# Kernel optimization log

Measured on AMD Instinct MI355X. Metric: run time of the kernel, lower is better.

The kernel has to match this reference:

```python
import jax, jax.numpy as jnp
import numpy as np

N, D = 131072, 512

def setup_inputs() -> dict:
    key = jax.random.key(0)
    k1, k2, k3 = jax.random.split(key, 3)
    feature = jax.random.normal(k1, (N, D), dtype=jnp.float32)
    mean = jax.random.normal(k2, (D,), dtype=jnp.float32)
    inverse_cov = jax.random.normal(k3, (D, D), dtype=jnp.float32)
    return {"feature": feature, "mean": mean, "inverse_cov": inverse_cov}

def reference(feature, mean, inverse_cov):
    # zero_f: [N, D]
    zero_f = feature - mean
    # diag(zero_f @ inv_cov @ zero_f.T) == rowwise quadratic form,
    # computed without the NxN intermediate: (zero_f @ inv_cov * zero_f).sum(-1)
    quad = jnp.einsum('nd,de,ne->n', zero_f, inverse_cov, zero_f)
    return jnp.mean(quad)
```

## Files before the change

kernel.cpp:

```cpp
#include <hip/hip_runtime.h>
#include <hip/hip_bf16.h>
#include <stdint.h>


typedef __attribute__((ext_vector_type(8))) short short8;
typedef __attribute__((ext_vector_type(4))) short short4v;
typedef __attribute__((ext_vector_type(4))) float floatx4;

static constexpr int NROWS = 131072;
static constexpr int DDIM  = 512;
static constexpr int AST   = 72;
static constexpr int SLOT  = 128 * AST;

__device__ __forceinline__ short f2bf(float f) {
  __bf16 b = (__bf16)f;
  return __builtin_bit_cast(short, b);
}
__device__ __forceinline__ float bf2f(short s) {
  __bf16 b = __builtin_bit_cast(__bf16, s);
  return (float)b;
}

__global__ __launch_bounds__(512) void maha_zero(float* __restrict__ s_ws,
                                                 float* __restrict__ out) {
  s_ws[threadIdx.x] = 0.0f;
  if (threadIdx.x == 0) out[0] = 0.0f;
}

__global__ __launch_bounds__(256, 2) void maha_gram(const float* __restrict__ F,
                                                    const float* __restrict__ C,
                                                    float* __restrict__ s_ws,
                                                    float* __restrict__ out) {
  __shared__ short As[2 * SLOT];
  __shared__ short Bs[2 * SLOT];
  __shared__ float sred[512];
  __shared__ float red[4];

  static const int TI[10] = {0,0,0,0,1,1,1,2,2,3};
  static const int TJ[10] = {0,1,2,3,1,2,3,2,3,3};

  const int bid  = blockIdx.x;
  const int gg   = bid / 80;
  const int rr   = bid % 80;
  const int slab = gg * 8 + (rr & 7);
  const int tile = rr >> 3;
  const int ti = TI[tile], tj = TJ[tile];
  const bool diag = (ti == tj);

  const int th = threadIdx.x;
  const int half = th >> 7;
  const int t2   = th & 127;
  const int tp   = t2 & 31;
  const int tn   = t2 >> 5;
  const int colbase = 128 * (half ? tj : ti);
  short* mybuf = half ? Bs : As;

  const int noff = (tn + (tp >> 2)) & 3;
  const int tphi = tp >> 4;
  const int gsw  = 8 * (tp & 7);

  const float* gbase = F + (size_t)slab * 1024 * DDIM + colbase + 4 * tp;

  floatx4 v[4][4];

  auto loadG = [&](int c) {
#pragma unroll
    for (int k = 0; k < 4; k++) {
      const int kq = k ^ tphi;
      const int nb = 4 * kq + noff;
      const float* p = gbase + (size_t)(c * 64 + 4 * nb) * DDIM;
#pragma unroll
      for (int nn = 0; nn < 4; nn++)
        v[k][nn] = *(const floatx4*)(p + nn * DDIM);
    }
  };

  float s_part[4] = {0.f, 0.f, 0.f, 0.f};
  const bool sacc = diag && (half == 0);

  auto cvtwrite = [&](int slot) {
#pragma unroll
    for (int k = 0; k < 4; k++) {
      const int kq = k ^ tphi;
      const int nb = 4 * kq + noff;
      const int naddr = (4 * nb) ^ gsw;
#pragma unroll
      for (int dd = 0; dd < 4; dd++) {
        short4v pk;
        pk[0] = f2bf(v[k][0][dd]); pk[1] = f2bf(v[k][1][dd]);
        pk[2] = f2bf(v[k][2][dd]); pk[3] = f2bf(v[k][3][dd]);
        *(short4v*)&mybuf[slot * SLOT + (4 * tp + dd) * AST + naddr] = pk;
        if (sacc)
          s_part[dd] += bf2f(pk[0]) + bf2f(pk[1]) + bf2f(pk[2]) + bf2f(pk[3]);
      }
    }
  };

  const int wave = th >> 6, lane = th & 63;
  const int wm = wave >> 1, wn = wave & 1;
  const int l15 = lane & 15, quad = lane >> 4;

  int aoff[4], swA[4], boff[4], swB[4];
#pragma unroll
  for (int mi = 0; mi < 4; mi++) {
    const int d = wm * 64 + mi * 16 + l15;
    aoff[mi] = d * AST;  swA[mi] = 8 * ((d >> 2) & 7);
    const int e = wn * 64 + mi * 16 + l15;
    boff[mi] = e * AST;  swB[mi] = 8 * ((e >> 2) & 7);
  }

  floatx4 acc[4][4];
#pragma unroll
  for (int i = 0; i < 4; i++)
#pragma unroll
    for (int j = 0; j < 4; j++) acc[i][j] = floatx4{0.f, 0.f, 0.f, 0.f};

  loadG(0);
  cvtwrite(0);
  loadG(1);

#pragma unroll 2
  for (int c = 0; c < 16; ++c) {
    const int slot = c & 1;
    __syncthreads();
    short8 af[2][4], bfr[2][4];
#pragma unroll
    for (int ks = 0; ks < 2; ks++) {
#pragma unroll
      for (int mi = 0; mi < 4; mi++)
        af[ks][mi] = *(const short8*)&As[slot * SLOT + aoff[mi] +
                                         ((ks * 32 + quad * 8) ^ swA[mi])];
#pragma unroll
      for (int fj = 0; fj < 4; fj++)
        bfr[ks][fj] = *(const short8*)&Bs[slot * SLOT + boff[fj] +
                                          ((ks * 32 + quad * 8) ^ swB[fj])];
    }
    if (c < 15) cvtwrite(slot ^ 1);
    if (c < 14) loadG(c + 2);
#pragma unroll
    for (int ks = 0; ks < 2; ks++)
#pragma unroll
      for (int mi = 0; mi < 4; mi++)
#pragma unroll
        for (int fj = 0; fj < 4; fj++)
          acc[mi][fj] = __builtin_amdgcn_mfma_f32_16x16x32_bf16(
              af[ks][mi], bfr[ks][fj], acc[mi][fj], 0, 0, 0);
  }

  const int d0 = ti * 128, e0 = tj * 128;
  float psum = 0.f;
#pragma unroll
  for (int mi = 0; mi < 4; mi++) {
#pragma unroll
    for (int fj = 0; fj < 4; fj++) {
      const int dg = d0 + wm * 64 + mi * 16 + quad * 4;
      const int eg = e0 + wn * 64 + fj * 16 + l15;
#pragma unroll
      for (int r2 = 0; r2 < 4; r2++) {
        float wgt = C[(size_t)(dg + r2) * DDIM + eg];
        if (!diag) wgt += C[(size_t)eg * DDIM + dg + r2];
        psum += wgt * acc[mi][fj][r2];
      }
    }
  }

#pragma unroll
  for (int off = 32; off > 0; off >>= 1) psum += __shfl_down(psum, off);
  if (lane == 0) red[wave] = psum;
  if (sacc) {
#pragma unroll
    for (int dd = 0; dd < 4; dd++) sred[(4 * tp + dd) * 4 + tn] = s_part[dd];
  }
  __syncthreads();
  if (th == 0) {
    const float tot = red[0] + red[1] + red[2] + red[3];
    atomicAdd(out, tot * (1.0f / (float)NROWS));
  }
  if (diag && th < 128) {
    const float sd = sred[th * 4] + sred[th * 4 + 1] + sred[th * 4 + 2] + sred[th * 4 + 3];
    atomicAdd(&s_ws[ti * 128 + th], sd);
  }
}

__global__ __launch_bounds__(256) void maha_corr(const float* __restrict__ C,
                                                 const float* __restrict__ mu,
                                                 const float* __restrict__ s_ws,
                                                 float* __restrict__ out) {
  __shared__ float red[4];
  const int b = blockIdx.x;
  const int th = threadIdx.x;
  float cd[4], md[4];
#pragma unroll
  for (int dd = 0; dd < 4; dd++) {
    const int d = b * 4 + dd;
    md[dd] = mu[d];
    cd[dd] = s_ws[d] - 0.5f * (float)NROWS * md[dd];
  }
  float p = 0.f;
#pragma unroll
  for (int rep = 0; rep < 2; rep++) {
    const int e = th + rep * 256;
    const float me = mu[e];
    const float ce = s_ws[e] - 0.5f * (float)NROWS * me;
#pragma unroll
    for (int dd = 0; dd < 4; dd++)
      p += C[(size_t)(b * 4 + dd) * DDIM + e] * (cd[dd] * me + md[dd] * ce);
  }
  const int lane = th & 63, wave = th >> 6;
#pragma unroll
  for (int off = 32; off > 0; off >>= 1) p += __shfl_down(p, off);
  if (lane == 0) red[wave] = p;
  __syncthreads();
  if (th == 0)
    atomicAdd(out, -(red[0] + red[1] + red[2] + red[3]) * (1.0f / (float)NROWS));
}

extern "C" void kernel_launch(void* const* d_in, const int* in_sizes, int n_in,
                              void* d_out, int out_size, void* d_ws, size_t ws_size,
                              hipStream_t stream) {
  const float* feature = (const float*)d_in[0];
  const float* mean    = (const float*)d_in[1];
  const float* invcov  = (const float*)d_in[2];
  float* out = (float*)d_out;
  float* s_ws = (float*)d_ws;

  maha_zero<<<1, 512, 0, stream>>>(s_ws, out);
  maha_gram<<<1280, 256, 0, stream>>>(feature, invcov, s_ws, out);
  maha_corr<<<128, 256, 0, stream>>>(invcov, mean, s_ws, out);
}
```

Measured before the change: 426.3 us.

## Split K across waves with 512-thread blocks and reuse A tile on diagonal

The Gram-tile kernel moves to 512 threads per block. The extra waves split each 64-wide K chunk between wave pairs, so each wave issues half the MFMAs and half the LDS fragment loads per iteration, and per-thread staging registers are halved. On diagonal tiles the B half of the block skips its global loads and conversions and reads from the A buffer instead, which cuts redundant feature traffic. The cost is more threads per block, a reduction over 8 waves, and a higher occupancy target that may force register spilling.

```diff
diff --git a/kernel.cpp b/kernel.cpp
--- a/kernel.cpp
+++ b/kernel.cpp
@@ -27,14 +27,13 @@
   if (threadIdx.x == 0) out[0] = 0.0f;
 }
 
-__global__ __launch_bounds__(256, 2) void maha_gram(const float* __restrict__ F,
+__global__ __launch_bounds__(512, 4) void maha_gram(const float* __restrict__ F,
                                                     const float* __restrict__ C,
                                                     float* __restrict__ s_ws,
                                                     float* __restrict__ out) {
-  __shared__ short As[2 * SLOT];
-  __shared__ short Bs[2 * SLOT];
-  __shared__ float sred[512];
-  __shared__ float red[4];
+  __shared__ short ABs[4 * SLOT];
+  __shared__ float sred[1024];
+  __shared__ float red[8];
 
   static const int TI[10] = {0,0,0,0,1,1,1,2,2,3};
   static const int TJ[10] = {0,1,2,3,1,2,3,2,3,3};
@@ -48,26 +47,28 @@
   const bool diag = (ti == tj);
 
   const int th = threadIdx.x;
-  const int half = th >> 7;
-  const int t2   = th & 127;
+  const int half = th >> 8;
+  const int t2   = th & 255;
   const int tp   = t2 & 31;
   const int tn   = t2 >> 5;
   const int colbase = 128 * (half ? tj : ti);
-  short* mybuf = half ? Bs : As;
-
-  const int noff = (tn + (tp >> 2)) & 3;
-  const int tphi = tp >> 4;
+  short* mybuf = ABs + (half ? 2 * SLOT : 0);
+  const bool skipstage = diag && (half == 1);
+
+  const int tphi = (tp >> 4) & 1;
+  const int noff = (tn + (tp >> 2)) & 7;
   const int gsw  = 8 * (tp & 7);
 
   const float* gbase = F + (size_t)slab * 1024 * DDIM + colbase + 4 * tp;
 
-  floatx4 v[4][4];
+  floatx4 v[2][4];
 
   auto loadG = [&](int c) {
-#pragma unroll
-    for (int k = 0; k < 4; k++) {
+    if (skipstage) return;
+#pragma unroll
+    for (int k = 0; k < 2; k++) {
       const int kq = k ^ tphi;
-      const int nb = 4 * kq + noff;
+      const int nb = 8 * kq + noff;
       const float* p = gbase + (size_t)(c * 64 + 4 * nb) * DDIM;
 #pragma unroll
       for (int nn = 0; nn < 4; nn++)
@@ -79,10 +80,11 @@
   const bool sacc = diag && (half == 0);
 
   auto cvtwrite = [&](int slot) {
-#pragma unroll
-    for (int k = 0; k < 4; k++) {
+    if (skipstage) return;
+#pragma unroll
+    for (int k = 0; k < 2; k++) {
       const int kq = k ^ tphi;
-      const int nb = 4 * kq + noff;
+      const int nb = 8 * kq + noff;
       const int naddr = (4 * nb) ^ gsw;
 #pragma unroll
       for (int dd = 0; dd < 4; dd++) {
@@ -97,8 +99,14 @@
   };
 
   const int wave = th >> 6, lane = th & 63;
-  const int wm = wave >> 1, wn = wave & 1;
+  const int wk = wave & 1;
+  const int wm = (wave >> 1) & 1;
+  const int wn = (wave >> 2) & 1;
   const int l15 = lane & 15, quad = lane >> 4;
+  const int kcol = wk * 32 + quad * 8;
+
+  const short* Ard = ABs;
+  const short* Brd = ABs + (diag ? 0 : 2 * SLOT);
 
   int aoff[4], swA[4], boff[4], swB[4];
 #pragma unroll
@@ -123,28 +131,21 @@
   for (int c = 0; c < 16; ++c) {
     const int slot = c & 1;
     __syncthreads();
-    short8 af[2][4], bfr[2][4];
-#pragma unroll
-    for (int ks = 0; ks < 2; ks++) {
-#pragma unroll
-      for (int mi = 0; mi < 4; mi++)
-        af[ks][mi] = *(const short8*)&As[slot * SLOT + aoff[mi] +
-                                         ((ks * 32 + quad * 8) ^ swA[mi])];
-#pragma unroll
-      for (int fj = 0; fj < 4; fj++)
-        bfr[ks][fj] = *(const short8*)&Bs[slot * SLOT + boff[fj] +
-                                          ((ks * 32 + quad * 8) ^ swB[fj])];
-    }
+    short8 af[4], bfr[4];
+#pragma unroll
+    for (int mi = 0; mi < 4; mi++)
+      af[mi] = *(const short8*)&Ard[slot * SLOT + aoff[mi] + (kcol ^ swA[mi])];
+#pragma unroll
+    for (int fj = 0; fj < 4; fj++)
+      bfr[fj] = *(const short8*)&Brd[slot * SLOT + boff[fj] + (kcol ^ swB[fj])];
     if (c < 15) cvtwrite(slot ^ 1);
     if (c < 14) loadG(c + 2);
 #pragma unroll
-    for (int ks = 0; ks < 2; ks++)
-#pragma unroll
-      for (int mi = 0; mi < 4; mi++)
-#pragma unroll
-        for (int fj = 0; fj < 4; fj++)
-          acc[mi][fj] = __builtin_amdgcn_mfma_f32_16x16x32_bf16(
-              af[ks][mi], bfr[ks][fj], acc[mi][fj], 0, 0, 0);
+    for (int mi = 0; mi < 4; mi++)
+#pragma unroll
+      for (int fj = 0; fj < 4; fj++)
+        acc[mi][fj] = __builtin_amdgcn_mfma_f32_16x16x32_bf16(
+            af[mi], bfr[fj], acc[mi][fj], 0, 0, 0);
   }
 
   const int d0 = ti * 128, e0 = tj * 128;
@@ -169,15 +170,18 @@
   if (lane == 0) red[wave] = psum;
   if (sacc) {
 #pragma unroll
-    for (int dd = 0; dd < 4; dd++) sred[(4 * tp + dd) * 4 + tn] = s_part[dd];
+    for (int dd = 0; dd < 4; dd++) sred[(4 * tp + dd) * 8 + tn] = s_part[dd];
   }
   __syncthreads();
   if (th == 0) {
-    const float tot = red[0] + red[1] + red[2] + red[3];
+    const float tot = red[0] + red[1] + red[2] + red[3] +
+                      red[4] + red[5] + red[6] + red[7];
     atomicAdd(out, tot * (1.0f / (float)NROWS));
   }
   if (diag && th < 128) {
-    const float sd = sred[th * 4] + sred[th * 4 + 1] + sred[th * 4 + 2] + sred[th * 4 + 3];
+    float sd = 0.f;
+#pragma unroll
+    for (int j = 0; j < 8; j++) sd += sred[th * 8 + j];
     atomicAdd(&s_ws[ti * 128 + th], sd);
   }
 }
@@ -225,6 +229,6 @@
   float* s_ws = (float*)d_ws;
 
   maha_zero<<<1, 512, 0, stream>>>(s_ws, out);
-  maha_gram<<<1280, 256, 0, stream>>>(feature, invcov, s_ws, out);
+  maha_gram<<<1280, 512, 0, stream>>>(feature, invcov, s_ws, out);
   maha_corr<<<128, 256, 0, stream>>>(invcov, mean, s_ws, out);
 }
```

After: 741.0 us. +73.8%, slower.
